# Kernel optimization log

Measured on AMD Instinct MI355X. Metric: run time of the kernel, lower is better.

The kernel has to match this reference:

```python
import jax, jax.numpy as jnp
import numpy as np

D = 1024
H = 16
K = D // H
B = 2
S = 2048

def setup_inputs() -> dict:
    key = jax.random.key(0)
    k1, k2, k3, k4, k5 = jax.random.split(key, 5)
    x = jax.random.normal(k1, (B, S, D), dtype=jnp.float32)
    # nn.Linear(d, 3d): weight [3d, d], bias [3d]
    Wqkv = jax.random.normal(k2, (3 * D, D), dtype=jnp.float32) / np.sqrt(D)
    bqkv = jax.random.normal(k3, (3 * D,), dtype=jnp.float32) * 0.01
    Wproj = jax.random.normal(k4, (D, D), dtype=jnp.float32) / np.sqrt(D)
    bproj = jax.random.normal(k5, (D,), dtype=jnp.float32) * 0.01
    return {"x": x, "Wqkv": Wqkv, "bqkv": bqkv, "Wproj": Wproj, "bproj": bproj}

def reference(x, Wqkv, bqkv, Wproj, bproj):
    Bsz, Slen, d = x.shape
    # fused QKV projection: [B,S,3d] -> [B,S,3,H,K] -> (3, B, H, S, K)
    qkv = (jnp.einsum('bsd,ed->bse', x, Wqkv) + bqkv).reshape(Bsz, Slen, 3, H, K)
    q, k, v = jnp.moveaxis(qkv, 2, 0).transpose(0, 1, 3, 2, 4)
    scale = 1.0 / jnp.sqrt(jnp.asarray(K, dtype=x.dtype))
    scores = jnp.einsum('bhqk,bhmk->bhqm', q, k) * scale  # [B,H,S,S]
    a = jax.nn.softmax(scores, axis=-1)
    # dropout is identity in eval mode
    o = jnp.einsum('bhqm,bhmk->bhqk', a, v)  # [B,H,S,K]
    o = o.transpose(0, 2, 1, 3).reshape(Bsz, Slen, d)
    return jnp.einsum('bsd,ed->bse', o, Wproj) + bproj
```

## Files before the change

kernel.cpp:

```cpp
#include <hip/hip_runtime.h>
#include <cstdint>

typedef unsigned short ushort_t;
typedef short short8 __attribute__((ext_vector_type(8)));
typedef float f32x4 __attribute__((ext_vector_type(4)));
typedef float float4v __attribute__((ext_vector_type(4)));
typedef unsigned int uint2v __attribute__((ext_vector_type(2)));

#define DDIM 1024
#define HH 16
#define HEADK 64
#define BB 2
#define SS 2048

#if __has_builtin(__builtin_amdgcn_exp2f)
#define EXP2F(x) __builtin_amdgcn_exp2f(x)
#else
#define EXP2F(x) exp2f(x)
#endif

__device__ __forceinline__ ushort_t f2bf(float f) {
  union { float f; uint32_t u; } c; c.f = f;
  uint32_t u = c.u;
  u += 0x7fffu + ((u >> 16) & 1u);
  return (ushort_t)(u >> 16);
}

__device__ __forceinline__ uint32_t pkbf_trunc(float a, float b) {
  union { float f; uint32_t u; } ca, cb;
  ca.f = a; cb.f = b;
  return __builtin_amdgcn_perm(cb.u, ca.u, 0x07060302);
}

__device__ __forceinline__ uint32_t pkbf_rne(float a, float b) {
  return (uint32_t)f2bf(a) | ((uint32_t)f2bf(b) << 16);
}

__device__ __forceinline__ float bfhi2f(uint32_t u) {
  union { uint32_t u; float f; } c; c.u = u & 0xffff0000u; return c.f;
}
__device__ __forceinline__ float bflo2f(uint32_t u) {
  union { uint32_t u; float f; } c; c.u = u << 16; return c.f;
}

__device__ __forceinline__ void glds16(const ushort_t* gp, ushort_t* lp) {
  __builtin_amdgcn_global_load_lds(
      (const __attribute__((address_space(1))) uint32_t*)gp,
      (__attribute__((address_space(3))) uint32_t*)lp, 16, 0, 0);
}

__global__ void cvt3_kernel(const float* __restrict__ s0, ushort_t* __restrict__ d0, int n0,
                            const float* __restrict__ s1, ushort_t* __restrict__ d1, int n1,
                            const float* __restrict__ s2, ushort_t* __restrict__ d2, int n2) {
  int i = blockIdx.x * blockDim.x + threadIdx.x;
  const float* src; ushort_t* dst; int k;
  if (i < n0) { src = s0; dst = d0; k = i; }
  else if (i < n0 + n1) { src = s1; dst = d1; k = i - n0; }
  else if (i < n0 + n1 + n2) { src = s2; dst = d2; k = i - n0 - n1; }
  else return;
  float4v v = ((const float4v*)src)[k];
  uint2v o; o[0] = pkbf_rne(v[0], v[1]); o[1] = pkbf_rne(v[2], v[3]);
  ((uint2v*)dst)[k] = o;
}

template <int MODE, int TM>
__global__ __launch_bounds__(256) void gemm_nt(
    const ushort_t* __restrict__ A, const ushort_t* __restrict__ Bm,
    const float* __restrict__ bias, float* __restrict__ Cout,
    ushort_t* __restrict__ Cbf, int M, int N, int Kd) {
  __shared__ ushort_t smem[128 * 64 * 2];
  ushort_t* As = smem;
  ushort_t* Bs = smem + TM * 64;
  const int MI = TM / 32;
  const int tid = threadIdx.x;
  const int wv = tid >> 6, lane = tid & 63;
  const int l15 = lane & 15, quad = lane >> 4;
  const int wm = wv >> 1, wn = wv & 1;
  const int tm0 = blockIdx.y * TM, tn0 = blockIdx.x * 128;

  f32x4 acc[MI][4];
#pragma unroll
  for (int i = 0; i < MI; ++i)
#pragma unroll
    for (int j = 0; j < 4; ++j) acc[i][j] = (f32x4){0.f, 0.f, 0.f, 0.f};

  const int lrow = lane >> 3;
  const int gcb = (lane & 7) ^ lrow;
  const int ACI = TM / 32;

  for (int k0 = 0; k0 < Kd; k0 += 64) {
#pragma unroll
    for (int c = 0; c < ACI; ++c) {
      int seg = wv * ACI + c;
      glds16(A + (size_t)(tm0 + seg * 8 + lrow) * Kd + k0 + gcb * 8,
             As + seg * 512);
    }
#pragma unroll
    for (int c = 0; c < 4; ++c) {
      int seg = wv * 4 + c;
      glds16(Bm + (size_t)(tn0 + seg * 8 + lrow) * Kd + k0 + gcb * 8,
             Bs + seg * 512);
    }
    __syncthreads();
#pragma unroll
    for (int kk = 0; kk < 64; kk += 32) {
      short8 af[MI], bfr[4];
#pragma unroll
      for (int i = 0; i < MI; ++i) {
        int r = wm * (TM / 2) + i * 16 + l15;
        int cb = (kk >> 3) + quad;
        af[i] = *(const short8*)(As + r * 64 + ((cb ^ (l15 & 7)) << 3));
      }
#pragma unroll
      for (int j = 0; j < 4; ++j) {
        int r = wn * 64 + j * 16 + l15;
        int cb = (kk >> 3) + quad;
        bfr[j] = *(const short8*)(Bs + r * 64 + ((cb ^ (l15 & 7)) << 3));
      }
#pragma unroll
      for (int i = 0; i < MI; ++i)
#pragma unroll
        for (int j = 0; j < 4; ++j)
          acc[i][j] = __builtin_amdgcn_mfma_f32_16x16x32_bf16(
              af[i], bfr[j], acc[i][j], 0, 0, 0);
    }
    __syncthreads();
  }

  if (MODE == 1) {
#pragma unroll
    for (int j = 0; j < 4; ++j) {
      int col = tn0 + wn * 64 + j * 16 + l15;
      float bv = bias[col];
#pragma unroll
      for (int i = 0; i < MI; ++i) {
        int row0 = tm0 + wm * (TM / 2) + i * 16 + quad * 4;
#pragma unroll
        for (int r = 0; r < 4; ++r)
          Cout[(size_t)(row0 + r) * N + col] = acc[i][j][r] + bv;
      }
    }
  } else {
    const int t = tn0 >> 10;
    if (t < 2) {
#pragma unroll
      for (int j = 0; j < 4; ++j) {
        int col = tn0 + wn * 64 + j * 16 + l15;
        float bv = bias[col];
        int hh = (col >> 6) & 15, kk2 = col & 63;
#pragma unroll
        for (int i = 0; i < MI; ++i) {
          int row0 = tm0 + wm * (TM / 2) + i * 16 + quad * 4;
#pragma unroll
          for (int r = 0; r < 4; ++r) {
            int row = row0 + r;
            int b = row >> 11, s = row & 2047;
            float v = acc[i][j][r] + bv;
            if (t == 0) v *= 0.18033688f;
            size_t base =
                (((size_t)t * BB + b) * HH + hh) * ((size_t)SS * HEADK);
            Cbf[base + (size_t)s * HEADK + kk2] = f2bf(v);
          }
        }
      }
    } else {
      __syncthreads();
#pragma unroll
      for (int j = 0; j < 4; ++j) {
        int c = wn * 64 + j * 16 + l15;
        float bv = bias[tn0 + c];
#pragma unroll
        for (int i = 0; i < MI; ++i) {
          int row0 = wm * (TM / 2) + i * 16 + quad * 4;
          uint2v dw;
          dw[0] = pkbf_rne(acc[i][j][0] + bv, acc[i][j][1] + bv);
          dw[1] = pkbf_rne(acc[i][j][2] + bv, acc[i][j][3] + bv);
          int rb = row0 >> 3;
          *(uint2v*)(&smem[c * 128 + (((rb ^ (c & 15)) << 3) | (row0 & 7))]) =
              dw;
        }
      }
      __syncthreads();
      const int rb2 = lane & 15;
      const int cg = lane >> 4;
#pragma unroll
      for (int it = 0; it < 8; ++it) {
        int c = wv * 32 + it * 4 + cg;
        short8 vv = *(const short8*)(&smem[c * 128 + ((rb2 ^ (c & 15)) << 3)]);
        int gcol = tn0 + c;
        int hh = (gcol >> 6) & 15, kk2 = gcol & 63;
        int grow = tm0 + rb2 * 8;
        int b = grow >> 11, s = grow & 2047;
        size_t base = (((size_t)2 * BB + b) * HH + hh) * ((size_t)SS * HEADK);
        *(short8*)(&Cbf[base + (size_t)kk2 * SS + s]) = vv;
      }
    }
  }
}

template <int NSPLIT>
__global__ __launch_bounds__(256, 4) void attn_kernel(
    const ushort_t* __restrict__ qkv, ushort_t* __restrict__ O0,
    ushort_t* __restrict__ O1, ushort_t* __restrict__ O2,
    ushort_t* __restrict__ O3, float* __restrict__ Lp) {
  constexpr int NT = (SS / NSPLIT) / 32;
  __shared__ ushort_t Kt[3][32 * 64];
  __shared__ ushort_t Vt[3][64 * 32];
  __shared__ ushort_t Pw[4][32 * 32];

  const int qt = blockIdx.x, h = blockIdx.y;
  const int b = blockIdx.z / NSPLIT, ns = blockIdx.z % NSPLIT;
  const int tid = threadIdx.x;
  const int wv = tid >> 6, lane = tid & 63;
  const int l15 = lane & 15, quad = lane >> 4;

  const size_t hstride = (size_t)SS * HEADK;
  const ushort_t* Qg = qkv + ((size_t)(0 * BB + b) * HH + h) * hstride;
  const ushort_t* Kg = qkv + ((size_t)(1 * BB + b) * HH + h) * hstride;
  const ushort_t* Vg = qkv + ((size_t)(2 * BB + b) * HH + h) * hstride;
  ushort_t* Opp;
  if (NSPLIT == 2) {
    Opp = ns ? O1 : O0;
  } else {
    Opp = (ns == 0) ? O0 : (ns == 1) ? O1 : (ns == 2) ? O2 : O3;
  }

  short8 qf[2][2];
#pragma unroll
  for (int mi = 0; mi < 2; ++mi)
#pragma unroll
    for (int kc = 0; kc < 2; ++kc)
      qf[mi][kc] = *(const short8*)(
          Qg + (size_t)(qt * 128 + wv * 32 + mi * 16 + l15) * 64 + kc * 32 +
          quad * 8);

  const short ONE = (short)0x3F80;
  short8 ones = {ONE, ONE, ONE, ONE, ONE, ONE, ONE, ONE};

  f32x4 oat[2][4];
  f32x4 loa[2];
#pragma unroll
  for (int mi = 0; mi < 2; ++mi) {
    loa[mi] = (f32x4){0.f, 0.f, 0.f, 0.f};
#pragma unroll
    for (int c = 0; c < 4; ++c) oat[mi][c] = (f32x4){0.f, 0.f, 0.f, 0.f};
  }

  const int lrow = lane >> 3, gcb = (lane & 7) ^ lrow;
  const int vfl = lane >> 2;
  const int vgb = (lane & 3) ^ ((vfl >> 1) & 3);

  const int pos0 = ns * (SS / NSPLIT);

  auto stage = [&](int jj, int db) {
    glds16(Kg + (size_t)(pos0 + jj * 32 + wv * 8 + lrow) * 64 + gcb * 8,
           &Kt[db][wv * 512]);
    glds16(Vg + (size_t)(wv * 16 + vfl) * SS + pos0 + jj * 32 + vgb * 8,
           &Vt[db][wv * 512]);
  };

  stage(0, 0);
  stage(1, 1);

  int cur = 0;
  for (int j = 0; j < NT; ++j) {
    if (j + 1 < NT)
      asm volatile("s_waitcnt vmcnt(2)" ::: "memory");
    else
      asm volatile("s_waitcnt vmcnt(0)" ::: "memory");
    __builtin_amdgcn_s_barrier();
    asm volatile("" ::: "memory");
    __builtin_amdgcn_sched_barrier(0);

    if (j + 2 < NT) {
      int tgt = cur + 2;
      if (tgt >= 3) tgt -= 3;
      stage(j + 2, tgt);
    }

    f32x4 st[2][2];
    __builtin_amdgcn_s_setprio(1);
#pragma unroll
    for (int cf = 0; cf < 2; ++cf) {
      int n = cf * 16 + l15;
      short8 kf0 = *(const short8*)(&Kt[cur][n * 64 + ((quad ^ (n & 7)) << 3)]);
      short8 kf1 =
          *(const short8*)(&Kt[cur][n * 64 + (((quad + 4) ^ (n & 7)) << 3)]);
#pragma unroll
      for (int mi = 0; mi < 2; ++mi) {
        f32x4 z = (f32x4){0.f, 0.f, 0.f, 0.f};
        z = __builtin_amdgcn_mfma_f32_16x16x32_bf16(kf0, qf[mi][0], z, 0, 0, 0);
        z = __builtin_amdgcn_mfma_f32_16x16x32_bf16(kf1, qf[mi][1], z, 0, 0, 0);
        st[mi][cf] = z;
      }
    }
    __builtin_amdgcn_s_setprio(0);

#pragma unroll
    for (int mi = 0; mi < 2; ++mi)
#pragma unroll
      for (int cf = 0; cf < 2; ++cf) {
        float e0 = EXP2F(st[mi][cf][0]);
        float e1 = EXP2F(st[mi][cf][1]);
        float e2 = EXP2F(st[mi][cf][2]);
        float e3 = EXP2F(st[mi][cf][3]);
        uint2v dw;
        dw[0] = pkbf_trunc(e0, e1);
        dw[1] = pkbf_trunc(e2, e3);
        int row = mi * 16 + l15;
        int pb = 2 * cf + (quad >> 1);
        int pbs = pb ^ ((l15 >> 1) & 3);
        *(uint2v*)(&Pw[wv][row * 32 + pbs * 8 + (quad & 1) * 4]) = dw;
      }

    short8 pa[2];
#pragma unroll
    for (int mi = 0; mi < 2; ++mi) {
      int row = mi * 16 + l15;
      pa[mi] = *(const short8*)(&Pw[wv][row * 32 +
                                        ((quad ^ ((l15 >> 1) & 3)) << 3)]);
    }

    __builtin_amdgcn_s_setprio(1);
#pragma unroll
    for (int cf = 0; cf < 4; ++cf) {
      short8 vf = *(const short8*)(&Vt[cur][(cf * 16 + l15) * 32 +
                                            ((quad ^ ((l15 >> 1) & 3)) << 3)]);
#pragma unroll
      for (int mi = 0; mi < 2; ++mi)
        oat[mi][cf] = __builtin_amdgcn_mfma_f32_16x16x32_bf16(
            vf, pa[mi], oat[mi][cf], 0, 0, 0);
    }
#pragma unroll
    for (int mi = 0; mi < 2; ++mi)
      loa[mi] = __builtin_amdgcn_mfma_f32_16x16x32_bf16(ones, pa[mi], loa[mi],
                                                        0, 0, 0);
    __builtin_amdgcn_s_setprio(0);

    cur = (cur == 2) ? 0 : cur + 1;
  }

  const size_t obase = ((size_t)b * HH + h) * SS * HEADK;
#pragma unroll
  for (int mi = 0; mi < 2; ++mi) {
#pragma unroll
    for (int cf = 0; cf < 4; ++cf) {
      uint2v dw;
      dw[0] = pkbf_rne(oat[mi][cf][0], oat[mi][cf][1]);
      dw[1] = pkbf_rne(oat[mi][cf][2], oat[mi][cf][3]);
      int cb = 2 * cf + (quad >> 1);
      int cbs = cb ^ (l15 & 7);
      *(uint2v*)(&Pw[wv][l15 * 64 + cbs * 8 + (quad & 1) * 4]) = dw;
    }
    const int r = lane >> 2;
#pragma unroll
    for (int pass = 0; pass < 2; ++pass) {
      int g = (lane & 3) + 4 * pass;
      short8 ov = *(const short8*)(&Pw[wv][r * 64 + ((g ^ (r & 7)) << 3)]);
      int qrow = qt * 128 + wv * 32 + mi * 16 + r;
      *(short8*)(&Opp[obase + (size_t)qrow * 64 + g * 8]) = ov;
    }
    if (quad == 0) {
      int qrow = qt * 128 + wv * 32 + mi * 16 + l15;
      Lp[((size_t)(ns * BB + b) * HH + h) * SS + qrow] = loa[mi][0];
    }
  }
}

template <int NSPLIT>
__global__ void reduce_kernel(const ushort_t* __restrict__ O0,
                              const ushort_t* __restrict__ O1,
                              const ushort_t* __restrict__ O2,
                              const ushort_t* __restrict__ O3,
                              const float* __restrict__ Lp,
                              ushort_t* __restrict__ ob) {
  const size_t nsL = (size_t)BB * HH * SS;
  int c = blockIdx.x * blockDim.x + threadIdx.x;
  int fc = c & 7;
  int hh = (c >> 3) & 15;
  int row = c >> 7;
  int b = row >> 11, s = row & 2047;
  size_t po = (((size_t)b * HH + hh) * SS + s) * 64 + fc * 8;
  size_t lo = ((size_t)b * HH + hh) * SS + s;
  const ushort_t* Ops[4] = {O0, O1, O2, O3};
  float acc[8];
#pragma unroll
  for (int i = 0; i < 8; ++i) acc[i] = 0.f;
  float l = 0.f;
#pragma unroll
  for (int t = 0; t < NSPLIT; ++t) {
    uint2v a0 = *(const uint2v*)(&Ops[t][po]);
    uint2v a1 = *(const uint2v*)(&Ops[t][po + 4]);
    acc[0] += bflo2f(a0[0]); acc[1] += bfhi2f(a0[0]);
    acc[2] += bflo2f(a0[1]); acc[3] += bfhi2f(a0[1]);
    acc[4] += bflo2f(a1[0]); acc[5] += bfhi2f(a1[0]);
    acc[6] += bflo2f(a1[1]); acc[7] += bfhi2f(a1[1]);
    l += Lp[(size_t)t * nsL + lo];
  }
  float inv = 1.0f / l;
  uint2v o0, o1;
  o0[0] = pkbf_rne(acc[0] * inv, acc[1] * inv);
  o0[1] = pkbf_rne(acc[2] * inv, acc[3] * inv);
  o1[0] = pkbf_rne(acc[4] * inv, acc[5] * inv);
  o1[1] = pkbf_rne(acc[6] * inv, acc[7] * inv);
  size_t oo = ((size_t)(b * SS + s)) * DDIM + hh * 64 + fc * 8;
  *(uint2v*)(&ob[oo]) = o0;
  *(uint2v*)(&ob[oo + 4]) = o1;
}

extern "C" void kernel_launch(void* const* d_in, const int* in_sizes, int n_in,
                              void* d_out, int out_size, void* d_ws,
                              size_t ws_size, hipStream_t stream) {
  const float* x = (const float*)d_in[0];
  const float* Wqkv = (const float*)d_in[1];
  const float* bqkv = (const float*)d_in[2];
  const float* Wproj = (const float*)d_in[3];
  const float* bproj = (const float*)d_in[4];
  float* out = (float*)d_out;

  ushort_t* xb = (ushort_t*)d_ws;
  ushort_t* wqb = xb + (size_t)4096 * 1024;
  ushort_t* wpb = wqb + (size_t)3072 * 1024;
  ushort_t* qkvb = wpb + (size_t)1024 * 1024;
  ushort_t* Op1 = qkvb + (size_t)3 * BB * HH * SS * HEADK;
  ushort_t* Op2 = Op1 + (size_t)BB * HH * SS * HEADK;
  ushort_t* Op3 = Op2 + (size_t)BB * HH * SS * HEADK;
  ushort_t* Op0 = xb;
  float* Lp = (float*)wqb;
  ushort_t* obuf = qkvb;

  const int n0 = 4096 * 1024 / 4, n1 = 3072 * 1024 / 4, n2 = 1024 * 1024 / 4;
  cvt3_kernel<<<(n0 + n1 + n2 + 255) / 256, 256, 0, stream>>>(
      x, xb, n0, Wqkv, wqb, n1, Wproj, wpb, n2);
  gemm_nt<0, 128><<<dim3(3072 / 128, 4096 / 128), 256, 0, stream>>>(
      xb, wqb, bqkv, nullptr, qkvb, 4096, 3072, 1024);

  const size_t need4 = 67108864ull;
  if (ws_size >= need4) {
    attn_kernel<4><<<dim3(16, 16, BB * 4), 256, 0, stream>>>(qkvb, Op0, Op1,
                                                             Op2, Op3, Lp);
    reduce_kernel<4><<<(BB * SS * DDIM / 8) / 256, 256, 0, stream>>>(
        Op0, Op1, Op2, Op3, Lp, obuf);
  } else {
    attn_kernel<2><<<dim3(16, 16, BB * 2), 256, 0, stream>>>(qkvb, Op0, Op1,
                                                             Op1, Op1, Lp);
    reduce_kernel<2><<<(BB * SS * DDIM / 8) / 256, 256, 0, stream>>>(
        Op0, Op1, Op1, Op1, Lp, obuf);
  }
  gemm_nt<1, 64><<<dim3(1024 / 128, 4096 / 64), 256, 0, stream>>>(
      obuf, wpb, bproj, out, nullptr, 4096, 1024, 1024);
}
```

Baseline: 195.4 us.

## Software-pipeline QK^T one tile ahead of PV and fix KV split at two

```diff
diff --git a/kernel.cpp b/kernel.cpp
--- a/kernel.cpp
+++ b/kernel.cpp
@@ -201,12 +201,11 @@
 template <int NSPLIT>
 __global__ __launch_bounds__(256, 4) void attn_kernel(
     const ushort_t* __restrict__ qkv, ushort_t* __restrict__ O0,
-    ushort_t* __restrict__ O1, ushort_t* __restrict__ O2,
-    ushort_t* __restrict__ O3, float* __restrict__ Lp) {
+    ushort_t* __restrict__ O1, float* __restrict__ Lp) {
   constexpr int NT = (SS / NSPLIT) / 32;
   __shared__ ushort_t Kt[3][32 * 64];
   __shared__ ushort_t Vt[3][64 * 32];
-  __shared__ ushort_t Pw[4][32 * 32];
+  __shared__ ushort_t Pw[4][2][32 * 32];
 
   const int qt = blockIdx.x, h = blockIdx.y;
   const int b = blockIdx.z / NSPLIT, ns = blockIdx.z % NSPLIT;
@@ -218,12 +217,7 @@
   const ushort_t* Qg = qkv + ((size_t)(0 * BB + b) * HH + h) * hstride;
   const ushort_t* Kg = qkv + ((size_t)(1 * BB + b) * HH + h) * hstride;
   const ushort_t* Vg = qkv + ((size_t)(2 * BB + b) * HH + h) * hstride;
-  ushort_t* Opp;
-  if (NSPLIT == 2) {
-    Opp = ns ? O1 : O0;
-  } else {
-    Opp = (ns == 0) ? O0 : (ns == 1) ? O1 : (ns == 2) ? O2 : O3;
-  }
+  ushort_t* Opp = ns ? O1 : O0;
 
   short8 qf[2][2];
 #pragma unroll
@@ -259,33 +253,15 @@
            &Vt[db][wv * 512]);
   };
 
-  stage(0, 0);
-  stage(1, 1);
-
-  int cur = 0;
-  for (int j = 0; j < NT; ++j) {
-    if (j + 1 < NT)
-      asm volatile("s_waitcnt vmcnt(2)" ::: "memory");
-    else
-      asm volatile("s_waitcnt vmcnt(0)" ::: "memory");
-    __builtin_amdgcn_s_barrier();
-    asm volatile("" ::: "memory");
-    __builtin_amdgcn_sched_barrier(0);
-
-    if (j + 2 < NT) {
-      int tgt = cur + 2;
-      if (tgt >= 3) tgt -= 3;
-      stage(j + 2, tgt);
-    }
-
+  auto qk_phase = [&](int kb, int pb) {
     f32x4 st[2][2];
     __builtin_amdgcn_s_setprio(1);
 #pragma unroll
     for (int cf = 0; cf < 2; ++cf) {
       int n = cf * 16 + l15;
-      short8 kf0 = *(const short8*)(&Kt[cur][n * 64 + ((quad ^ (n & 7)) << 3)]);
+      short8 kf0 = *(const short8*)(&Kt[kb][n * 64 + ((quad ^ (n & 7)) << 3)]);
       short8 kf1 =
-          *(const short8*)(&Kt[cur][n * 64 + (((quad + 4) ^ (n & 7)) << 3)]);
+          *(const short8*)(&Kt[kb][n * 64 + (((quad + 4) ^ (n & 7)) << 3)]);
 #pragma unroll
       for (int mi = 0; mi < 2; ++mi) {
         f32x4 z = (f32x4){0.f, 0.f, 0.f, 0.f};
@@ -295,7 +271,6 @@
       }
     }
     __builtin_amdgcn_s_setprio(0);
-
 #pragma unroll
     for (int mi = 0; mi < 2; ++mi)
 #pragma unroll
@@ -308,24 +283,45 @@
         dw[0] = pkbf_trunc(e0, e1);
         dw[1] = pkbf_trunc(e2, e3);
         int row = mi * 16 + l15;
-        int pb = 2 * cf + (quad >> 1);
-        int pbs = pb ^ ((l15 >> 1) & 3);
-        *(uint2v*)(&Pw[wv][row * 32 + pbs * 8 + (quad & 1) * 4]) = dw;
-      }
+        int pbv = 2 * cf + (quad >> 1);
+        int pbs = pbv ^ ((l15 >> 1) & 3);
+        *(uint2v*)(&Pw[wv][pb][row * 32 + pbs * 8 + (quad & 1) * 4]) = dw;
+      }
+  };
+
+  stage(0, 0);
+  stage(1, 1);
+
+  asm volatile("s_waitcnt vmcnt(2)" ::: "memory");
+  __builtin_amdgcn_s_barrier();
+  asm volatile("" ::: "memory");
+  __builtin_amdgcn_sched_barrier(0);
+  qk_phase(0, 0);
+
+  int vb = 0;
+  for (int j = 0; j < NT; ++j) {
+    const int kb = (vb == 2) ? 0 : vb + 1;
+    const int sb = (kb == 2) ? 0 : kb + 1;
+    asm volatile("s_waitcnt vmcnt(0)" ::: "memory");
+    __builtin_amdgcn_s_barrier();
+    asm volatile("" ::: "memory");
+    __builtin_amdgcn_sched_barrier(0);
+
+    if (j + 2 < NT) stage(j + 2, sb);
+    if (j + 1 < NT) qk_phase(kb, (j + 1) & 1);
 
     short8 pa[2];
 #pragma unroll
     for (int mi = 0; mi < 2; ++mi) {
       int row = mi * 16 + l15;
-      pa[mi] = *(const short8*)(&Pw[wv][row * 32 +
-                                        ((quad ^ ((l15 >> 1) & 3)) << 3)]);
-    }
-
+      pa[mi] = *(const short8*)(&Pw[wv][j & 1][row * 32 +
+                                              ((quad ^ ((l15 >> 1) & 3)) << 3)]);
+    }
     __builtin_amdgcn_s_setprio(1);
 #pragma unroll
     for (int cf = 0; cf < 4; ++cf) {
-      short8 vf = *(const short8*)(&Vt[cur][(cf * 16 + l15) * 32 +
-                                            ((quad ^ ((l15 >> 1) & 3)) << 3)]);
+      short8 vf = *(const short8*)(&Vt[vb][(cf * 16 + l15) * 32 +
+                                           ((quad ^ ((l15 >> 1) & 3)) << 3)]);
 #pragma unroll
       for (int mi = 0; mi < 2; ++mi)
         oat[mi][cf] = __builtin_amdgcn_mfma_f32_16x16x32_bf16(
@@ -337,7 +333,7 @@
                                                         0, 0, 0);
     __builtin_amdgcn_s_setprio(0);
 
-    cur = (cur == 2) ? 0 : cur + 1;
+    vb = kb;
   }
 
   const size_t obase = ((size_t)b * HH + h) * SS * HEADK;
@@ -350,13 +346,13 @@
       dw[1] = pkbf_rne(oat[mi][cf][2], oat[mi][cf][3]);
       int cb = 2 * cf + (quad >> 1);
       int cbs = cb ^ (l15 & 7);
-      *(uint2v*)(&Pw[wv][l15 * 64 + cbs * 8 + (quad & 1) * 4]) = dw;
+      *(uint2v*)(&Pw[wv][0][l15 * 64 + cbs * 8 + (quad & 1) * 4]) = dw;
     }
     const int r = lane >> 2;
 #pragma unroll
     for (int pass = 0; pass < 2; ++pass) {
       int g = (lane & 3) + 4 * pass;
-      short8 ov = *(const short8*)(&Pw[wv][r * 64 + ((g ^ (r & 7)) << 3)]);
+      short8 ov = *(const short8*)(&Pw[wv][0][r * 64 + ((g ^ (r & 7)) << 3)]);
       int qrow = qt * 128 + wv * 32 + mi * 16 + r;
       *(short8*)(&Opp[obase + (size_t)qrow * 64 + g * 8]) = ov;
     }
@@ -370,8 +366,6 @@
 template <int NSPLIT>
 __global__ void reduce_kernel(const ushort_t* __restrict__ O0,
                               const ushort_t* __restrict__ O1,
-                              const ushort_t* __restrict__ O2,
-                              const ushort_t* __restrict__ O3,
                               const float* __restrict__ Lp,
                               ushort_t* __restrict__ ob) {
   const size_t nsL = (size_t)BB * HH * SS;
@@ -382,7 +376,7 @@
   int b = row >> 11, s = row & 2047;
   size_t po = (((size_t)b * HH + hh) * SS + s) * 64 + fc * 8;
   size_t lo = ((size_t)b * HH + hh) * SS + s;
-  const ushort_t* Ops[4] = {O0, O1, O2, O3};
+  const ushort_t* Ops[2] = {O0, O1};
   float acc[8];
 #pragma unroll
   for (int i = 0; i < 8; ++i) acc[i] = 0.f;
@@ -423,8 +417,6 @@
   ushort_t* wpb = wqb + (size_t)3072 * 1024;
   ushort_t* qkvb = wpb + (size_t)1024 * 1024;
   ushort_t* Op1 = qkvb + (size_t)3 * BB * HH * SS * HEADK;
-  ushort_t* Op2 = Op1 + (size_t)BB * HH * SS * HEADK;
-  ushort_t* Op3 = Op2 + (size_t)BB * HH * SS * HEADK;
   ushort_t* Op0 = xb;
   float* Lp = (float*)wqb;
   ushort_t* obuf = qkvb;
@@ -434,19 +426,9 @@
       x, xb, n0, Wqkv, wqb, n1, Wproj, wpb, n2);
   gemm_nt<0, 128><<<dim3(3072 / 128, 4096 / 128), 256, 0, stream>>>(
       xb, wqb, bqkv, nullptr, qkvb, 4096, 3072, 1024);
-
-  const size_t need4 = 67108864ull;
-  if (ws_size >= need4) {
-    attn_kernel<4><<<dim3(16, 16, BB * 4), 256, 0, stream>>>(qkvb, Op0, Op1,
-                                                             Op2, Op3, Lp);
-    reduce_kernel<4><<<(BB * SS * DDIM / 8) / 256, 256, 0, stream>>>(
-        Op0, Op1, Op2, Op3, Lp, obuf);
-  } else {
-    attn_kernel<2><<<dim3(16, 16, BB * 2), 256, 0, stream>>>(qkvb, Op0, Op1,
-                                                             Op1, Op1, Lp);
-    reduce_kernel<2><<<(BB * SS * DDIM / 8) / 256, 256, 0, stream>>>(
-        Op0, Op1, Op1, Op1, Lp, obuf);
-  }
+  attn_kernel<2><<<dim3(16, 16, BB * 2), 256, 0, stream>>>(qkvb, Op0, Op1, Lp);
+  reduce_kernel<2><<<(BB * SS * DDIM / 8) / 256, 256, 0, stream>>>(Op0, Op1,
+                                                                   Lp, obuf);
   gemm_nt<1, 64><<<dim3(1024 / 128, 4096 / 64), 256, 0, stream>>>(
       obuf, wpb, bproj, out, nullptr, 4096, 1024, 1024);
 }
```

Result: no change. 193.4 us (-1.0%).
